# Kernel tuning notes

Hardware: AMD Instinct MI355X
Metric: run time of the kernel (lower is better)

## Reference

```python
import jax, jax.numpy as jnp
import numpy as np
from jax import lax
from jax.scipy.special import erf

EPS = 1e-5
B = 256

def _conv(x, w, stride):
    return lax.conv_general_dilated(x, w, (stride, stride), ((1, 1), (1, 1)),
                                    dimension_numbers=('NCHW', 'OIHW', 'NCHW'))

def lr_conv(x, alpha, betta, bias, stride):
    # Ternary weight distribution (LR-nets): p0 = P(w=0), p1 = P(w=1)
    p0 = jax.nn.sigmoid(alpha)
    p1 = (1.0 - p0) * jax.nn.sigmoid(betta)
    w_mean = 2.0 * p1 + p0 - 1.0          # E[w] = p1 - p_{-1}
    w_var = (1.0 - p0) - w_mean * w_mean  # Var[w] = E[w^2] - E[w]^2
    m = _conv(x, w_mean, stride) + bias[None, :, None, None]
    v = _conv(x * x, w_var, stride)
    return m, v

def sign_prob(m, v):
    # expected sign under CLT Gaussian: 2*Phi(m/sqrt(v)) - 1 = erf(m / sqrt(2 v))
    return erf(m / jnp.sqrt(2.0 * (v + EPS)))

def setup_inputs() -> dict:
    key = jax.random.key(0)
    ks = jax.random.split(key, 32)
    def n(k, shape, s=1.0):
        return jax.random.normal(k, shape, dtype=jnp.float32) * s
    inp = {}
    inp['x'] = n(ks[0], (B, 3, 32, 32))
    shapes = [(128, 3), (128, 128), (256, 128), (256, 256), (512, 256), (512, 512)]
    i = 1
    for li, (co, ci) in enumerate(shapes, start=1):
        inp['a%d' % li] = n(ks[i], (co, ci, 3, 3)); i += 1
        inp['b%d' % li] = n(ks[i], (co, ci, 3, 3)); i += 1
        inp['c%d' % li] = jnp.zeros((co,), jnp.float32)
    inp['bn_gamma'] = jnp.ones((512,), jnp.float32)
    inp['bn_beta'] = jnp.zeros((512,), jnp.float32)
    inp['fc1_w'] = n(ks[20], (1024, 8192), 0.01)
    inp['fc1_b'] = jnp.zeros((1024,), jnp.float32)
    inp['fc2_w'] = n(ks[21], (10, 1024), 0.03)
    inp['fc2_b'] = jnp.zeros((10,), jnp.float32)
    inp['noise6'] = n(ks[22], (B, 512, 4, 4))
    return inp

def reference(x, a1, b1, c1, a2, b2, c2, a3, b3, c3, a4, b4, c4, a5, b5, c5,
              a6, b6, c6, bn_gamma, bn_beta, fc1_w, fc1_b, fc2_w, fc2_b, noise6):
    h = x
    for (a, bt, c, s) in [(a1, b1, c1, 1), (a2, b2, c2, 2), (a3, b3, c3, 1),
                          (a4, b4, c4, 2), (a5, b5, c5, 1)]:
        m, v = lr_conv(h, a, bt, c, s)
        h = sign_prob(m, v)
    m, v = lr_conv(h, a6, b6, c6, 2)          # output_sample=True layer
    z = m + jnp.sqrt(v + EPS) * noise6        # reparameterized Gaussian sample
    mu = jnp.mean(z, axis=(0, 2, 3), keepdims=True)
    var = jnp.var(z, axis=(0, 2, 3), keepdims=True)
    z = bn_gamma[None, :, None, None] * (z - mu) / jnp.sqrt(var + EPS) + bn_beta[None, :, None, None]
    z = jax.nn.relu(z).reshape(z.shape[0], -1)  # [B, 8192]
    z = jax.nn.relu(z @ fc1_w.T + fc1_b)
    return z @ fc2_w.T + fc2_b
```

## Files before the change

### kernel.cpp

```cpp
#include <hip/hip_runtime.h>
#include <hip/hip_bf16.h>
#include <math.h>

#define EPS 1e-5f

typedef __hip_bfloat16 bf16;
typedef short s16x8 __attribute__((ext_vector_type(8)));
typedef float f32x4 __attribute__((ext_vector_type(4)));

constexpr int ilog2c(int v) { return v <= 1 ? 0 : 1 + ilog2c(v >> 1); }

__device__ __forceinline__ float ldin(const void* p, size_t i, int isbf) {
    return isbf ? __bfloat162float(((const bf16*)p)[i]) : ((const float*)p)[i];
}
__device__ __forceinline__ float b2f_bits(short s) {
    unsigned u = ((unsigned)(unsigned short)s) << 16;
    return __builtin_bit_cast(float, u);
}
__device__ __forceinline__ uint4 sqpk4(uint4 u) {
    uint4 r;
    unsigned* up = (unsigned*)&u;
    unsigned* rp = (unsigned*)&r;
#pragma unroll
    for (int k = 0; k < 4; k++) {
        unsigned w = up[k];
        float lo = __builtin_bit_cast(float, w << 16);
        float hi = __builtin_bit_cast(float, w & 0xffff0000u);
        lo *= lo; hi *= hi;
        unsigned ul = __builtin_bit_cast(unsigned, lo) + 0x8000u;
        unsigned uh = __builtin_bit_cast(unsigned, hi) + 0x8000u;
        rp[k] = (ul >> 16) | (uh & 0xffff0000u);
    }
    return r;
}

__device__ __forceinline__ void dma16(const void* g, void* l) {
    __builtin_amdgcn_global_load_lds(
        (const __attribute__((address_space(1))) void*)g,
        (__attribute__((address_space(3))) void*)l, 16, 0, 0);
}

__global__ __launch_bounds__(64) void detect_kernel(const void* __restrict__ x,
                                                    int* __restrict__ flags,
                                                    char* __restrict__ gA,
                                                    char* __restrict__ gB) {
    const unsigned* w = (const unsigned*)x;
    unsigned word = w[threadIdx.x];
    int e = (word >> 23) & 0xFF;
    bool ok = (word == 0u) || (e >= 0x70 && e <= 0x8E);
    unsigned long long m = __ballot(ok);
    if (threadIdx.x == 0) flags[0] = (__popcll(m) >= 32) ? 0 : 1;
    if (threadIdx.x < 16) ((uint4*)gA)[threadIdx.x] = (uint4){0, 0, 0, 0};
    else if (threadIdx.x < 32) ((uint4*)gB)[threadIdx.x - 16] = (uint4){0, 0, 0, 0};
}

__global__ __launch_bounds__(256) void prep_w_l1(
    const void* __restrict__ alpha, const void* __restrict__ betta,
    const int* __restrict__ flags, float* __restrict__ wmv, int n)
{
    int i = blockIdx.x * 256 + threadIdx.x;
    if (i >= n) return;
    int fl = flags[0];
    float a = ldin(alpha, i, fl), b = ldin(betta, i, fl);
    float p0 = 1.f / (1.f + expf(-a));
    float p1 = (1.f - p0) / (1.f + expf(-b));
    float m = 2.f * p1 + p0 - 1.f;
    wmv[i] = m;
    wmv[n + i] = (1.f - p0) - m * m;
}

__global__ __launch_bounds__(256) void prep_w_r(
    const void* __restrict__ alpha, const void* __restrict__ betta,
    const int* __restrict__ flags, bf16* __restrict__ wmr, bf16* __restrict__ wvr,
    int lc, int n)
{
    int o = blockIdx.x * 256 + threadIdx.x;
    if (o >= n) return;
    int fl = flags[0];
    int cotap = o >> lc;
    int ci = o & ((1 << lc) - 1);
    int co = cotap / 9;
    int tap = cotap - co * 9;
    int i = (((co << lc) + ci) * 9) + tap;
    float a = ldin(alpha, i, fl), b = ldin(betta, i, fl);
    float p0 = 1.f / (1.f + expf(-a));
    float p1 = (1.f - p0) / (1.f + expf(-b));
    float m = 2.f * p1 + p0 - 1.f;
    float v = (1.f - p0) - m * m;
    wmr[o] = __float2bfloat16(m);
    wvr[o] = __float2bfloat16(v);
}

__global__ __launch_bounds__(256) void permute_fc1(
    const void* __restrict__ w, const int* __restrict__ flags, bf16* __restrict__ wp)
{
    __shared__ float L[8192];
    const int fl = flags[0];
    int tid = threadIdx.x;
    int o = blockIdx.x;
    size_t srow = (size_t)o * 8192;
    for (int c = tid; c < 512; c += 256) {
        float v[16];
        if (fl) {
            const uint4* s = (const uint4*)((const bf16*)w + srow + c * 16);
            uint4 u0 = s[0], u1 = s[1];
            const unsigned short* h0 = (const unsigned short*)&u0;
            const unsigned short* h1 = (const unsigned short*)&u1;
#pragma unroll
            for (int j = 0; j < 8; j++) { v[j] = b2f_bits((short)h0[j]); v[8 + j] = b2f_bits((short)h1[j]); }
        } else {
            const float4* s = (const float4*)((const float*)w + srow + c * 16);
#pragma unroll
            for (int j = 0; j < 4; j++) {
                float4 t4 = s[j];
                v[j * 4 + 0] = t4.x; v[j * 4 + 1] = t4.y; v[j * 4 + 2] = t4.z; v[j * 4 + 3] = t4.w;
            }
        }
#pragma unroll
        for (int hw = 0; hw < 16; hw++) L[hw * 512 + c] = v[hw];
    }
    __syncthreads();
    for (int j = 0; j < 32; j++) {
        int idx = j * 256 + tid;
        wp[srow + idx] = __float2bfloat16(L[idx]);
    }
}

__global__ __launch_bounds__(256) void l1_conv(
    const void* __restrict__ x, const float* __restrict__ wmv,
    const void* __restrict__ bias, const int* __restrict__ flags,
    bf16* __restrict__ out)
{
    __shared__ float Xs[64][28];
    const int fl = flags[0];
    int tid = threadIdx.x;
    int pos0 = blockIdx.x * 64;
    int b = pos0 >> 10;
    for (int u = tid; u < 576; u += 256) {
        int p = u / 9, r = u - p * 9;
        int ci = r / 3, kh = r - ci * 3;
        int pos = pos0 + p;
        int oh = (pos >> 5) & 31, ow = pos & 31;
        int ih = oh - 1 + kh;
        bool okh = (unsigned)ih < 32u;
        size_t base = ((size_t)(b * 3 + ci) * 32 + ih) * 32;
#pragma unroll
        for (int kw = 0; kw < 3; kw++) {
            int iw = ow - 1 + kw;
            float v = (okh && (unsigned)iw < 32u) ? ldin(x, base + iw, fl) : 0.f;
            Xs[p][ci * 9 + kh * 3 + kw] = v;
        }
    }
    int c = tid & 127, pg = tid >> 7;
    float wm[27], wv[27];
#pragma unroll
    for (int k = 0; k < 27; k++) {
        wm[k] = wmv[c * 27 + k];
        wv[k] = wmv[3456 + c * 27 + k];
    }
    float bs = ldin(bias, c, fl);
    __syncthreads();
    for (int it = 0; it < 32; it++) {
        int p = it * 2 + pg;
        float aM = 0.f, aV = 0.f;
#pragma unroll
        for (int k = 0; k < 27; k++) {
            float xv = Xs[p][k];
            aM = fmaf(xv, wm[k], aM);
            aV = fmaf(xv * xv, wv[k], aV);
        }
        out[(size_t)(pos0 + p) * 128 + c] =
            __float2bfloat16(erff((aM + bs) * rsqrtf(2.f * (aV + EPS))));
    }
}

template<int CI, int CO, int H, int W, int S, int OH, int OW, int ACT, int SQX, int COT>
__global__ __launch_bounds__(256, 2) void conv_gemm(
    const char* __restrict__ xreg,
    int sqoff, int zpoff,
    const bf16* __restrict__ wmr,
    const bf16* __restrict__ wvr,
    const void* __restrict__ bias, const void* __restrict__ noise,
    const int* __restrict__ flags,
    void* __restrict__ outp, bf16* __restrict__ outsq)
{
    constexpr int OHW = OH * OW;
    constexpr int KC = CI / 64;
    constexpr int NC = 9 * KC;
    constexpr int WJ = COT / 32;
    constexpr int NIW = COT / 8;
    constexpr int LOHW = ilog2c(OHW), LOW = ilog2c(OW);
    constexpr int LH = ilog2c(H), LW = ilog2c(W);
    static_assert(COT == 128 || COT == 64, "");

    __shared__ bf16 Xs[128 * 64];
    __shared__ bf16 Xq[128 * 64];
    __shared__ bf16 Wms[COT * 64];
    __shared__ bf16 Wvs[COT * 64];

    const int tid = threadIdx.x;
    const int lane = tid & 63, wv_ = tid >> 6;
    const int q = lane >> 4, l15 = lane & 15;
    const int pw = (wv_ >> 1) * 64, cw = (wv_ & 1) * (16 * WJ);
    const int c0 = blockIdx.y * COT;
    const int bx128 = blockIdx.x * 128;

    const int lrow = lane >> 3;
    const int u16 = (((lane & 7) ^ lrow) << 4);

    const int wlb = ((c0 + lrow) * 9 * CI + (((lane & 7) ^ lrow) << 3)) * 2;

    const bf16* wsrc = (wv_ == 3) ? wvr : wmr;
    bf16* wdst = (wv_ == 3) ? Wvs : Wms;
    bf16* xdst = (wv_ == 1) ? Xq : Xs;
    const int xadd = (wv_ == 1) ? sqoff : 0;

    f32x4 accM[4][WJ], accV[4][WJ];
#pragma unroll
    for (int i = 0; i < 4; i++)
#pragma unroll
        for (int j = 0; j < WJ; j++) {
            accM[i][j] = (f32x4){0.f, 0.f, 0.f, 0.f};
            accV[i][j] = (f32x4){0.f, 0.f, 0.f, 0.f};
        }

    for (int t = 0; t < NC; t++) {
        const int tap = t / KC, ci0 = (t % KC) * 64;
        const int kh = tap / 3, kw = tap - 3 * kh;
        const int sci = ci0 * 2;

        __syncthreads();
        if (wv_ >= 2) {
            const int base = wlb + t * 128;
#pragma unroll
            for (int k = 0; k < NIW; k++)
                dma16((const char*)wsrc + base + k * (8 * 9 * CI * 2),
                      (char*)wdst + k * 1024);
        } else {
            if constexpr (!SQX) {
#pragma unroll
                for (int k = 0; k < 16; k++) {
                    int P = bx128 + 8 * k + lrow;
                    int bi = P >> LOHW;
                    int oh = (P >> LOW) & (OH - 1);
                    int ow = P & (OW - 1);
                    int ih = oh * S - 1 + kh;
                    int iw = ow * S - 1 + kw;
                    bool ok = ((unsigned)ih < (unsigned)H) && ((unsigned)iw < (unsigned)W);
                    int off = ((((bi << LH) + ih) << LW) + iw) * (CI * 2) + u16 + sci + xadd;
                    off = ok ? off : zpoff;
                    dma16(xreg + off, (char*)xdst + k * 1024);
                }
            } else {
#pragma unroll
                for (int ts = 0; ts < 8; ts++) {
                    int k = 2 * ts + wv_;
                    int P = bx128 + 8 * k + lrow;
                    int bi = P >> LOHW;
                    int oh = (P >> LOW) & (OH - 1);
                    int ow = P & (OW - 1);
                    int ih = oh * S - 1 + kh;
                    int iw = ow * S - 1 + kw;
                    bool ok = ((unsigned)ih < (unsigned)H) && ((unsigned)iw < (unsigned)W);
                    int off = ((((bi << LH) + ih) << LW) + iw) * (CI * 2) + u16 + sci;
                    uint4 g = (uint4){0, 0, 0, 0};
                    if (ok) g = *(const uint4*)(xreg + off);
                    *(uint4*)((char*)Xs + k * 1024 + lane * 16) = g;
                    *(uint4*)((char*)Xq + k * 1024 + lane * 16) = sqpk4(g);
                }
            }
        }
        __syncthreads();

#pragma unroll
        for (int ks = 0; ks < 2; ks++) {
            const int pu = (((ks * 4 + q) ^ (l15 & 7)) << 3);
            s16x8 a[4], aq[4];
#pragma unroll
            for (int i = 0; i < 4; i++) {
                const int ra = pw + i * 16 + l15;
                a[i]  = *(const s16x8*)(Xs + ra * 64 + pu);
                aq[i] = *(const s16x8*)(Xq + ra * 64 + pu);
            }
#pragma unroll
            for (int j = 0; j < WJ; j++) {
                const int rb = cw + j * 16 + l15;
                s16x8 bm = *(const s16x8*)(Wms + rb * 64 + pu);
                s16x8 bv = *(const s16x8*)(Wvs + rb * 64 + pu);
#pragma unroll
                for (int i = 0; i < 4; i++) {
                    accM[i][j] = __builtin_amdgcn_mfma_f32_16x16x32_bf16(a[i],  bm, accM[i][j], 0, 0, 0);
                    accV[i][j] = __builtin_amdgcn_mfma_f32_16x16x32_bf16(aq[i], bv, accV[i][j], 0, 0, 0);
                }
            }
        }
    }

    const int fl = flags[0];
#pragma unroll
    for (int j = 0; j < WJ; j++) {
        int co = c0 + cw + j * 16 + l15;
        float bs = ldin(bias, co, fl);
#pragma unroll
        for (int i = 0; i < 4; i++) {
            f32x4 m4 = accM[i][j], v4 = accV[i][j];
#pragma unroll
            for (int r = 0; r < 4; r++) {
                int PP = bx128 + pw + i * 16 + q * 4 + r;
                float mm = m4[r] + bs, vv = v4[r];
                if (ACT == 0) {
                    float y = erff(mm * rsqrtf(2.f * (vv + EPS)));
                    bf16 yb = __float2bfloat16(y);
                    ((bf16*)outp)[(size_t)PP * CO + co] = yb;
                    float yf = __bfloat162float(yb);
                    outsq[(size_t)PP * CO + co] = __float2bfloat16(yf * yf);
                } else {
                    int bb = PP / OHW, hw = PP % OHW;
                    float nz = ldin(noise, ((size_t)bb * CO + co) * OHW + hw, fl);
                    ((float*)outp)[(size_t)PP * CO + co] = mm + sqrtf(vv + EPS) * nz;
                }
            }
        }
    }
}

__global__ __launch_bounds__(256) void fc1_gemm_sk(
    const bf16* __restrict__ A, const bf16* __restrict__ Wp,
    float* __restrict__ part)
{
    __shared__ bf16 Xs[128 * 40];
    __shared__ bf16 Ws[128 * 40];
    int tid = threadIdx.x;
    int lane = tid & 63, wv_ = tid >> 6;
    int q = lane >> 4, l15 = lane & 15;
    const int pw = (wv_ >> 1) * 64, cw = (wv_ & 1) * 64;
    const int p0 = blockIdx.x * 128, c0 = blockIdx.y * 128;
    const int kb = blockIdx.z * 1024;
    const int row_i = tid >> 1, half = tid & 1;

    f32x4 acc[4][4];
#pragma unroll
    for (int i = 0; i < 4; i++)
#pragma unroll
        for (int j = 0; j < 4; j++) acc[i][j] = (f32x4){0.f, 0.f, 0.f, 0.f};

    for (int k0 = kb; k0 < kb + 1024; k0 += 32) {
        __syncthreads();
        {
            const uint4* s = (const uint4*)(A + (size_t)(p0 + row_i) * 8192 + k0 + half * 16);
            uint4* d = (uint4*)(Xs + row_i * 40 + half * 16);
            d[0] = s[0]; d[1] = s[1];
        }
        {
            const uint4* s = (const uint4*)(Wp + (size_t)(c0 + row_i) * 8192 + k0 + half * 16);
            uint4* d = (uint4*)(Ws + row_i * 40 + half * 16);
            d[0] = s[0]; d[1] = s[1];
        }
        __syncthreads();
        s16x8 a[4], bb[4];
#pragma unroll
        for (int i = 0; i < 4; i++) {
            a[i]  = *(const s16x8*)(Xs + (pw + i * 16 + l15) * 40 + q * 8);
            bb[i] = *(const s16x8*)(Ws + (cw + i * 16 + l15) * 40 + q * 8);
        }
#pragma unroll
        for (int i = 0; i < 4; i++)
#pragma unroll
            for (int j = 0; j < 4; j++)
                acc[i][j] = __builtin_amdgcn_mfma_f32_16x16x32_bf16(a[i], bb[j], acc[i][j], 0, 0, 0);
    }

    float* pbase = part + (size_t)blockIdx.z * 256 * 1024;
#pragma unroll
    for (int j = 0; j < 4; j++) {
        int co = c0 + cw + j * 16 + l15;
#pragma unroll
        for (int i = 0; i < 4; i++) {
            f32x4 m4 = acc[i][j];
#pragma unroll
            for (int r = 0; r < 4; r++) {
                int P = p0 + pw + i * 16 + q * 4 + r;
                pbase[(size_t)P * 1024 + co] = m4[r];
            }
        }
    }
}

__global__ __launch_bounds__(256) void fc1_reduce(
    const float* __restrict__ part, const void* __restrict__ bias,
    const int* __restrict__ flags, float* __restrict__ out)
{
    int i = blockIdx.x * 256 + threadIdx.x;
    float s = 0.f;
#pragma unroll
    for (int k = 0; k < 8; k++) s += part[(size_t)k * 262144 + i];
    out[i] = fmaxf(s + ldin(bias, i & 1023, flags[0]), 0.f);
}

__global__ __launch_bounds__(256) void bn_part(const float* __restrict__ z,
                                               float4* __restrict__ partial)
{
    int blk = blockIdx.x;
    int t = threadIdx.x;
    float s0 = 0, ss0 = 0, s1 = 0, ss1 = 0;
    for (int p = 0; p < 32; p++) {
        float2 v = ((const float2*)z)[((size_t)(blk * 32 + p)) * 256 + t];
        s0 += v.x; ss0 += v.x * v.x;
        s1 += v.y; ss1 += v.y * v.y;
    }
    partial[blk * 256 + t] = make_float4(s0, ss0, s1, ss1);
}

__global__ __launch_bounds__(512) void bn_fin(
    const float4* __restrict__ partial, const void* __restrict__ gamma,
    const void* __restrict__ beta, const int* __restrict__ flags,
    float* __restrict__ sc, float* __restrict__ sh)
{
    int c = threadIdx.x;
    float s = 0, ss = 0;
    for (int j = 0; j < 128; j++) {
        float4 pv = partial[j * 256 + (c >> 1)];
        s += (c & 1) ? pv.z : pv.x;
        ss += (c & 1) ? pv.w : pv.y;
    }
    float mean = s * (1.f / 4096.f);
    float var = ss * (1.f / 4096.f) - mean * mean;
    int fl = flags[0];
    float scale = ldin(gamma, c, fl) * rsqrtf(var + EPS);
    sc[c] = scale;
    sh[c] = ldin(beta, c, fl) - mean * scale;
}

__global__ __launch_bounds__(256) void bn_apply(
    const float* __restrict__ z, const float* __restrict__ sc,
    const float* __restrict__ sh, bf16* __restrict__ zr)
{
    int i = blockIdx.x * 256 + threadIdx.x;
    int c = i & 511;
    float v = z[i] * sc[c] + sh[c];
    zr[i] = __float2bfloat16(fmaxf(v, 0.f));
}

__global__ __launch_bounds__(640) void fc2_kernel(
    const float* __restrict__ A, const void* __restrict__ W,
    const void* __restrict__ bias, const int* __restrict__ flags,
    void* __restrict__ out)
{
    const int fl = flags[0];
    int n = blockIdx.x;
    int o = threadIdx.x >> 6;
    int lane = threadIdx.x & 63;
    const float* a = A + (size_t)n * 1024;
    size_t wbase = (size_t)o * 1024;
    float s = 0.f;
    for (int i = lane; i < 1024; i += 64) s = fmaf(a[i], ldin(W, wbase + i, fl), s);
#pragma unroll
    for (int off = 32; off > 0; off >>= 1) s += __shfl_down(s, off);
    if (lane == 0) {
        float v = s + ldin(bias, o, fl);
        if (fl) ((bf16*)out)[n * 10 + o] = __float2bfloat16(v);
        else    ((float*)out)[n * 10 + o] = v;
    }
}

extern "C" void kernel_launch(void* const* d_in, const int* in_sizes, int n_in,
                              void* d_out, int out_size, void* d_ws, size_t ws_size,
                              hipStream_t stream)
{
    const void* x = d_in[0];
    const void *al[6], *be[6], *bi[6];
    for (int l = 0; l < 6; l++) {
        al[l] = d_in[1 + 3 * l];
        be[l] = d_in[2 + 3 * l];
        bi[l] = d_in[3 + 3 * l];
    }
    const void* bn_gamma = d_in[19];
    const void* bn_beta  = d_in[20];
    const void* fc1_w = d_in[21];
    const void* fc1_b = d_in[22];
    const void* fc2_w = d_in[23];
    const void* fc2_b = d_in[24];
    const void* noise = d_in[25];

    char* base = (char*)d_ws;
    size_t off = 0;
    auto alloc = [&](size_t bytes) { void* p = base + off; off += (bytes + 255) & ~(size_t)255; return p; };
    int* flags = (int*)alloc(256);
    float* w1 = (float*)alloc(2 * 3456 * sizeof(float));
    const int SwLC[5] = {7, 7, 8, 8, 9};
    const size_t Sw[5] = {147456, 294912, 589824, 1179648, 2359296};
    bf16 *wmr[5], *wvr[5];
    for (int l = 0; l < 5; l++) {
        wmr[l] = (bf16*)alloc(Sw[l] * sizeof(bf16));
        wvr[l] = (bf16*)alloc(Sw[l] * sizeof(bf16));
    }
    bf16* Wp   = (bf16*)alloc((size_t)1024 * 8192 * sizeof(bf16));
    float4* part = (float4*)alloc((size_t)128 * 256 * sizeof(float4));
    float* bnsc = (float*)alloc(512 * sizeof(float));
    float* bnsh = (float*)alloc(512 * sizeof(float));
    float* fc1o = (float*)alloc((size_t)256 * 1024 * sizeof(float));
    bf16* zr   = (bf16*)alloc((size_t)256 * 8192 * sizeof(bf16));

    const int ZPA = 67108864;
    const int ZPB = 33554432;
    char* RA = (char*)alloc((size_t)ZPA + 256);
    char* RB = (char*)alloc((size_t)ZPB + 256);
    float* z = (float*)RB;
    float* fc1part = (float*)(RB + 8388608);

    detect_kernel<<<1, 64, 0, stream>>>(x, flags, RA + ZPA, RB + ZPB);

    prep_w_l1<<<14, 256, 0, stream>>>(al[0], be[0], flags, w1, 3456);
    for (int l = 0; l < 5; l++) {
        int n = (int)Sw[l];
        prep_w_r<<<(n + 255) / 256, 256, 0, stream>>>(
            al[l + 1], be[l + 1], flags, wmr[l], wvr[l], SwLC[l], n);
    }
    permute_fc1<<<1024, 256, 0, stream>>>(fc1_w, flags, Wp);

    l1_conv<<<4096, 256, 0, stream>>>(x, w1, bi[0], flags, (bf16*)RA);

    conv_gemm<128, 128, 32, 32, 2, 16, 16, 0, 1, 128><<<dim3(512, 1), 256, 0, stream>>>(
        RA, 0, ZPA, wmr[0], wvr[0], bi[1], nullptr, flags,
        RB, (bf16*)(RB + 16777216));
    conv_gemm<128, 256, 16, 16, 1, 16, 16, 0, 0, 128><<<dim3(512, 2), 256, 0, stream>>>(
        RB, 16777216, ZPB, wmr[1], wvr[1], bi[2], nullptr, flags,
        RA, (bf16*)(RA + 33554432));
    conv_gemm<256, 256, 16, 16, 2, 8, 8, 0, 0, 128><<<dim3(128, 2), 256, 0, stream>>>(
        RA, 33554432, ZPA, wmr[2], wvr[2], bi[3], nullptr, flags,
        RB, (bf16*)(RB + 8388608));
    conv_gemm<256, 512, 8, 8, 1, 8, 8, 0, 0, 128><<<dim3(128, 4), 256, 0, stream>>>(
        RB, 8388608, ZPB, wmr[3], wvr[3], bi[4], nullptr, flags,
        RA, (bf16*)(RA + 16777216));
    conv_gemm<512, 512, 8, 8, 2, 4, 4, 1, 0, 64><<<dim3(32, 8), 256, 0, stream>>>(
        RA, 16777216, ZPA, wmr[4], wvr[4], bi[5], noise, flags,
        z, nullptr);

    bn_part<<<128, 256, 0, stream>>>(z, part);
    bn_fin<<<1, 512, 0, stream>>>(part, bn_gamma, bn_beta, flags, bnsc, bnsh);
    bn_apply<<<8192, 256, 0, stream>>>(z, bnsc, bnsh, zr);

    fc1_gemm_sk<<<dim3(2, 8, 8), 256, 0, stream>>>(zr, Wp, fc1part);
    fc1_reduce<<<1024, 256, 0, stream>>>(fc1part, fc1_b, flags, fc1o);
    fc2_kernel<<<256, 640, 0, stream>>>(fc1o, fc2_w, fc2_b, flags, d_out);
}
```

Before: 781.1 us.

## Double-buffer conv GEMM K-chunks and stage activation epilogue through LDS

Makes the conv GEMM K loop use 32-channel chunks with double-buffered LDS, so the next tile's global/DMA loads are issued before computing the current one and one barrier per iteration is removed. Per-row position offsets are precomputed once instead of every chunk. For the erf activation path, outputs are first written to LDS and then stored as coalesced 16-byte rows instead of scattered 2-byte stores. The costs are twice as many loop iterations with half-K MFMA work per barrier, more registers held for prefetch, and the same LDS footprint, which may affect occupancy at two blocks per CU.

```diff
diff --git a/kernel.cpp b/kernel.cpp
--- a/kernel.cpp
+++ b/kernel.cpp
@@ -185,18 +185,22 @@
     void* __restrict__ outp, bf16* __restrict__ outsq)
 {
     constexpr int OHW = OH * OW;
-    constexpr int KC = CI / 64;
+    constexpr int KC = CI / 32;
     constexpr int NC = 9 * KC;
     constexpr int WJ = COT / 32;
-    constexpr int NIW = COT / 8;
+    constexpr int NW = COT / 16;
+    constexpr int XB = 128 * 64;
+    constexpr int WB = COT * 64;
     constexpr int LOHW = ilog2c(OHW), LOW = ilog2c(OW);
     constexpr int LH = ilog2c(H), LW = ilog2c(W);
-    static_assert(COT == 128 || COT == 64, "");
-
-    __shared__ bf16 Xs[128 * 64];
-    __shared__ bf16 Xq[128 * 64];
-    __shared__ bf16 Wms[COT * 64];
-    __shared__ bf16 Wvs[COT * 64];
+    constexpr int SMEM = 4 * XB + 4 * WB;
+    static_assert(ACT == 1 || COT == 128, "LDS epilogue assumes 256B rows");
+
+    __shared__ __align__(16) char smem[SMEM];
+    char* const Xs0 = smem;
+    char* const Xq0 = smem + 2 * XB;
+    char* const Wm0 = smem + 4 * XB;
+    char* const Wv0 = smem + 4 * XB + 2 * WB;
 
     const int tid = threadIdx.x;
     const int lane = tid & 63, wv_ = tid >> 6;
@@ -205,15 +209,19 @@
     const int c0 = blockIdx.y * COT;
     const int bx128 = blockIdx.x * 128;
 
-    const int lrow = lane >> 3;
-    const int u16 = (((lane & 7) ^ lrow) << 4);
-
-    const int wlb = ((c0 + lrow) * 9 * CI + (((lane & 7) ^ lrow) << 3)) * 2;
-
-    const bf16* wsrc = (wv_ == 3) ? wvr : wmr;
-    bf16* wdst = (wv_ == 3) ? Wvs : Wms;
-    bf16* xdst = (wv_ == 1) ? Xq : Xs;
-    const int xadd = (wv_ == 1) ? sqoff : 0;
+    const int lrow = lane >> 2;
+    const int u16 = (((lane & 3) ^ (lrow & 3)) << 4);
+
+    int xb[8], ohS[8], owS[8];
+#pragma unroll
+    for (int k = 0; k < 8; k++) {
+        int P = bx128 + 16 * k + lrow;
+        int bi = P >> LOHW;
+        ohS[k] = ((P >> LOW) & (OH - 1)) * S - 1;
+        owS[k] = (P & (OW - 1)) * S - 1;
+        xb[k] = bi * (H * W * CI * 2);
+    }
+    const int wlb = ((c0 + lrow) * 9 * CI) * 2 + u16;
 
     f32x4 accM[4][WJ], accV[4][WJ];
 #pragma unroll
@@ -224,97 +232,145 @@
             accV[i][j] = (f32x4){0.f, 0.f, 0.f, 0.f};
         }
 
+    uint4 g[4];
+
+    auto stageW = [&](int t, int nb) {
+        const int tap = t / KC, ci = (t - tap * KC) * 32;
+        const char* src = (const char*)((wv_ == 3) ? wvr : wmr) + wlb + (tap * CI + ci) * 2;
+        char* dst = ((wv_ == 3) ? Wv0 : Wm0) + nb * WB;
+#pragma unroll
+        for (int k = 0; k < NW; k++)
+            dma16(src + k * (16 * 9 * CI * 2), dst + k * 1024);
+    };
+
+    auto stageX = [&](int t, int nb) {
+        const int tap = t / KC, ci = (t - tap * KC) * 32;
+        const int kh = tap / 3, kw = tap - 3 * kh;
+        char* dst = ((wv_ == 1) ? Xq0 : Xs0) + nb * XB;
+        const int xadd = (wv_ == 1) ? sqoff : 0;
+#pragma unroll
+        for (int k = 0; k < 8; k++) {
+            int ih = ohS[k] + kh, iw = owS[k] + kw;
+            bool ok = ((unsigned)ih < (unsigned)H) && ((unsigned)iw < (unsigned)W);
+            int off = xb[k] + (ih * W + iw) * (CI * 2) + u16 + ci * 2 + xadd;
+            off = ok ? off : zpoff;
+            dma16(xreg + off, dst + k * 1024);
+        }
+    };
+
+    auto loadX = [&](int t) {
+        const int tap = t / KC, ci = (t - tap * KC) * 32;
+        const int kh = tap / 3, kw = tap - 3 * kh;
+#pragma unroll
+        for (int ts = 0; ts < 4; ts++) {
+            const int k = 2 * ts + wv_;
+            int ih = ohS[k] + kh, iw = owS[k] + kw;
+            bool ok = ((unsigned)ih < (unsigned)H) && ((unsigned)iw < (unsigned)W);
+            int off = xb[k] + (ih * W + iw) * (CI * 2) + u16 + ci * 2;
+            g[ts] = (uint4){0, 0, 0, 0};
+            if (ok) g[ts] = *(const uint4*)(xreg + off);
+        }
+    };
+    auto writeX = [&](int nb) {
+#pragma unroll
+        for (int ts = 0; ts < 4; ts++) {
+            const int k = 2 * ts + wv_;
+            *(uint4*)(Xs0 + nb * XB + k * 1024 + lane * 16) = g[ts];
+            *(uint4*)(Xq0 + nb * XB + k * 1024 + lane * 16) = sqpk4(g[ts]);
+        }
+    };
+
+    auto compute = [&](int nb) {
+        const bf16* Xs = (const bf16*)(Xs0 + nb * XB);
+        const bf16* Xq = (const bf16*)(Xq0 + nb * XB);
+        const bf16* Wm = (const bf16*)(Wm0 + nb * WB);
+        const bf16* Wv = (const bf16*)(Wv0 + nb * WB);
+        const int pu = (q ^ (l15 & 3)) << 3;
+        s16x8 a[4], aq[4];
+#pragma unroll
+        for (int i = 0; i < 4; i++) {
+            const int ra = pw + i * 16 + l15;
+            a[i]  = *(const s16x8*)(Xs + ra * 32 + pu);
+            aq[i] = *(const s16x8*)(Xq + ra * 32 + pu);
+        }
+#pragma unroll
+        for (int j = 0; j < WJ; j++) {
+            const int rb = cw + j * 16 + l15;
+            s16x8 bm = *(const s16x8*)(Wm + rb * 32 + pu);
+            s16x8 bv = *(const s16x8*)(Wv + rb * 32 + pu);
+#pragma unroll
+            for (int i = 0; i < 4; i++) {
+                accM[i][j] = __builtin_amdgcn_mfma_f32_16x16x32_bf16(a[i],  bm, accM[i][j], 0, 0, 0);
+                accV[i][j] = __builtin_amdgcn_mfma_f32_16x16x32_bf16(aq[i], bv, accV[i][j], 0, 0, 0);
+            }
+        }
+    };
+
+    if (wv_ >= 2) stageW(0, 0);
+    else if constexpr (!SQX) stageX(0, 0);
+    else { loadX(0); writeX(0); }
+    __syncthreads();
+
+#pragma unroll 2
     for (int t = 0; t < NC; t++) {
-        const int tap = t / KC, ci0 = (t % KC) * 64;
-        const int kh = tap / 3, kw = tap - 3 * kh;
-        const int sci = ci0 * 2;
-
+        const int cur = t & 1;
+        const bool more = (t + 1 < NC);
+        if (more) {
+            if (wv_ >= 2) stageW(t + 1, cur ^ 1);
+            else if constexpr (!SQX) stageX(t + 1, cur ^ 1);
+            else loadX(t + 1);
+        }
+        compute(cur);
+        if constexpr (SQX) { if (wv_ < 2 && more) writeX(cur ^ 1); }
         __syncthreads();
-        if (wv_ >= 2) {
-            const int base = wlb + t * 128;
-#pragma unroll
-            for (int k = 0; k < NIW; k++)
-                dma16((const char*)wsrc + base + k * (8 * 9 * CI * 2),
-                      (char*)wdst + k * 1024);
-        } else {
-            if constexpr (!SQX) {
-#pragma unroll
-                for (int k = 0; k < 16; k++) {
-                    int P = bx128 + 8 * k + lrow;
-                    int bi = P >> LOHW;
-                    int oh = (P >> LOW) & (OH - 1);
-                    int ow = P & (OW - 1);
-                    int ih = oh * S - 1 + kh;
-                    int iw = ow * S - 1 + kw;
-                    bool ok = ((unsigned)ih < (unsigned)H) && ((unsigned)iw < (unsigned)W);
-                    int off = ((((bi << LH) + ih) << LW) + iw) * (CI * 2) + u16 + sci + xadd;
-                    off = ok ? off : zpoff;
-                    dma16(xreg + off, (char*)xdst + k * 1024);
-                }
-            } else {
-#pragma unroll
-                for (int ts = 0; ts < 8; ts++) {
-                    int k = 2 * ts + wv_;
-                    int P = bx128 + 8 * k + lrow;
-                    int bi = P >> LOHW;
-                    int oh = (P >> LOW) & (OH - 1);
-                    int ow = P & (OW - 1);
-                    int ih = oh * S - 1 + kh;
-                    int iw = ow * S - 1 + kw;
-                    bool ok = ((unsigned)ih < (unsigned)H) && ((unsigned)iw < (unsigned)W);
-                    int off = ((((bi << LH) + ih) << LW) + iw) * (CI * 2) + u16 + sci;
-                    uint4 g = (uint4){0, 0, 0, 0};
-                    if (ok) g = *(const uint4*)(xreg + off);
-                    *(uint4*)((char*)Xs + k * 1024 + lane * 16) = g;
-                    *(uint4*)((char*)Xq + k * 1024 + lane * 16) = sqpk4(g);
+    }
+
+    const int fl = flags[0];
+    if constexpr (ACT == 0) {
+        bf16* Lact = (bf16*)smem;
+        bf16* Lsq  = (bf16*)(smem + 128 * COT * 2);
+#pragma unroll
+        for (int j = 0; j < WJ; j++) {
+            int co = c0 + cw + j * 16 + l15;
+            float bs = ldin(bias, co, fl);
+#pragma unroll
+            for (int i = 0; i < 4; i++) {
+#pragma unroll
+                for (int r = 0; r < 4; r++) {
+                    int PPl = pw + i * 16 + q * 4 + r;
+                    float mm = accM[i][j][r] + bs, vv = accV[i][j][r];
+                    float y = erff(mm * rsqrtf(2.f * (vv + EPS)));
+                    bf16 yb = __float2bfloat16(y);
+                    float yf = __bfloat162float(yb);
+                    int lc = cw + j * 16 + l15;
+                    Lact[PPl * COT + lc] = yb;
+                    Lsq [PPl * COT + lc] = __float2bfloat16(yf * yf);
                 }
             }
         }
         __syncthreads();
-
-#pragma unroll
-        for (int ks = 0; ks < 2; ks++) {
-            const int pu = (((ks * 4 + q) ^ (l15 & 7)) << 3);
-            s16x8 a[4], aq[4];
+#pragma unroll
+        for (int k = 0; k < 8; k++) {
+            int f = k * 4096 + tid * 16;
+            int rowl = f >> 8;
+            int colb = f & 255;
+            uint4 va = *(const uint4*)((char*)Lact + f);
+            uint4 vs = *(const uint4*)((char*)Lsq + f);
+            size_t gb = ((size_t)(bx128 + rowl) * CO + c0) * 2 + colb;
+            *(uint4*)((char*)outp + gb) = va;
+            *(uint4*)((char*)outsq + gb) = vs;
+        }
+    } else {
+#pragma unroll
+        for (int j = 0; j < WJ; j++) {
+            int co = c0 + cw + j * 16 + l15;
+            float bs = ldin(bias, co, fl);
 #pragma unroll
             for (int i = 0; i < 4; i++) {
-                const int ra = pw + i * 16 + l15;
-                a[i]  = *(const s16x8*)(Xs + ra * 64 + pu);
-                aq[i] = *(const s16x8*)(Xq + ra * 64 + pu);
-            }
-#pragma unroll
-            for (int j = 0; j < WJ; j++) {
-                const int rb = cw + j * 16 + l15;
-                s16x8 bm = *(const s16x8*)(Wms + rb * 64 + pu);
-                s16x8 bv = *(const s16x8*)(Wvs + rb * 64 + pu);
-#pragma unroll
-                for (int i = 0; i < 4; i++) {
-                    accM[i][j] = __builtin_amdgcn_mfma_f32_16x16x32_bf16(a[i],  bm, accM[i][j], 0, 0, 0);
-                    accV[i][j] = __builtin_amdgcn_mfma_f32_16x16x32_bf16(aq[i], bv, accV[i][j], 0, 0, 0);
-                }
-            }
-        }
-    }
-
-    const int fl = flags[0];
-#pragma unroll
-    for (int j = 0; j < WJ; j++) {
-        int co = c0 + cw + j * 16 + l15;
-        float bs = ldin(bias, co, fl);
-#pragma unroll
-        for (int i = 0; i < 4; i++) {
-            f32x4 m4 = accM[i][j], v4 = accV[i][j];
-#pragma unroll
-            for (int r = 0; r < 4; r++) {
-                int PP = bx128 + pw + i * 16 + q * 4 + r;
-                float mm = m4[r] + bs, vv = v4[r];
-                if (ACT == 0) {
-                    float y = erff(mm * rsqrtf(2.f * (vv + EPS)));
-                    bf16 yb = __float2bfloat16(y);
-                    ((bf16*)outp)[(size_t)PP * CO + co] = yb;
-                    float yf = __bfloat162float(yb);
-                    outsq[(size_t)PP * CO + co] = __float2bfloat16(yf * yf);
-                } else {
+#pragma unroll
+                for (int r = 0; r < 4; r++) {
+                    int PP = bx128 + pw + i * 16 + q * 4 + r;
+                    float mm = accM[i][j][r] + bs, vv = accV[i][j][r];
                     int bb = PP / OHW, hw = PP % OHW;
                     float nz = ldin(noise, ((size_t)bb * CO + co) * OHW + hw, fl);
                     ((float*)outp)[(size_t)PP * CO + co] = mm + sqrtf(vv + EPS) * nz;
```

After: 755.4 us. 1.03x faster.

## Triple-buffer conv GEMM loads and compute squared activations in registers

Applied to the files above, without the earlier changes.

The conv GEMM now walks the K dimension in 32-channel chunks through a three-stage shared-memory ring. Async DMA of chunk t+2 overlaps MFMA on chunk t, with hand-placed waitcnt/barrier. The separate squared-activation tensor is dropped: x² is computed in registers from the loaded A fragments, which removes the extra global writes and reads of outsq. The activation epilogue is staged through LDS for coalesced 16-byte stores, and layer 3 switches to 64-channel tiles. This trades more LDS and hand-tuned wait counts, which could be fragile, for less memory traffic and better latency hiding.

```diff
diff --git a/kernel.cpp b/kernel.cpp
--- a/kernel.cpp
+++ b/kernel.cpp
@@ -174,29 +174,27 @@
     }
 }
 
-template<int CI, int CO, int H, int W, int S, int OH, int OW, int ACT, int SQX, int COT>
+template<int CI, int CO, int H, int W, int S, int OH, int OW, int ACT, int COT>
 __global__ __launch_bounds__(256, 2) void conv_gemm(
     const char* __restrict__ xreg,
-    int sqoff, int zpoff,
+    int zpoff,
     const bf16* __restrict__ wmr,
     const bf16* __restrict__ wvr,
     const void* __restrict__ bias, const void* __restrict__ noise,
-    const int* __restrict__ flags,
-    void* __restrict__ outp, bf16* __restrict__ outsq)
+    const int* __restrict__ flags, void* __restrict__ outp)
 {
     constexpr int OHW = OH * OW;
-    constexpr int KC = CI / 64;
+    constexpr int KC = CI / 32;
     constexpr int NC = 9 * KC;
     constexpr int WJ = COT / 32;
-    constexpr int NIW = COT / 8;
+    constexpr int NW = COT / 16;
+    constexpr int XB = 128 * 64;
+    constexpr int WB = COT * 64;
+    constexpr int BUFB = XB + 2 * WB;
     constexpr int LOHW = ilog2c(OHW), LOW = ilog2c(OW);
-    constexpr int LH = ilog2c(H), LW = ilog2c(W);
-    static_assert(COT == 128 || COT == 64, "");
-
-    __shared__ bf16 Xs[128 * 64];
-    __shared__ bf16 Xq[128 * 64];
-    __shared__ bf16 Wms[COT * 64];
-    __shared__ bf16 Wvs[COT * 64];
+    static_assert(NC % 3 == 0, "");
+
+    __shared__ __align__(16) char smem[3 * BUFB];
 
     const int tid = threadIdx.x;
     const int lane = tid & 63, wv_ = tid >> 6;
@@ -205,15 +203,26 @@
     const int c0 = blockIdx.y * COT;
     const int bx128 = blockIdx.x * 128;
 
-    const int lrow = lane >> 3;
-    const int u16 = (((lane & 7) ^ lrow) << 4);
-
-    const int wlb = ((c0 + lrow) * 9 * CI + (((lane & 7) ^ lrow) << 3)) * 2;
-
-    const bf16* wsrc = (wv_ == 3) ? wvr : wmr;
-    bf16* wdst = (wv_ == 3) ? Wvs : Wms;
-    bf16* xdst = (wv_ == 1) ? Xq : Xs;
-    const int xadd = (wv_ == 1) ? sqoff : 0;
+    const int sl   = (lane & 7) ^ (lane >> 3);
+    const int row2 = 2 * (lane >> 3) + (sl >> 2);
+    const int u16b = (sl & 3) * 16;
+
+    int xb[4], ohS[4], owS[4];
+#pragma unroll
+    for (int kk = 0; kk < 4; kk++) {
+        int P = bx128 + 16 * ((wv_ & 1) * 4 + kk) + row2;
+        int bi = P >> LOHW;
+        ohS[kk] = ((P >> LOW) & (OH - 1)) * S - 1;
+        owS[kk] = (P & (OW - 1)) * S - 1;
+        xb[kk] = bi * (H * W * CI * 2);
+    }
+    const char* wsb = (const char*)((wv_ == 3) ? wvr : wmr)
+                      + (size_t)(c0 + row2) * (9 * CI * 2) + u16b;
+    const int wdoff = XB + ((wv_ == 3) ? WB : 0);
+
+    const int lA = (l15 >> 1) * 128 + (((((l15 & 1) << 2) | q) ^ (l15 >> 1)) << 4);
+    const int abase = pw * 64 + lA;
+    const int bbase = cw * 64 + lA;
 
     f32x4 accM[4][WJ], accV[4][WJ];
 #pragma unroll
@@ -224,97 +233,111 @@
             accV[i][j] = (f32x4){0.f, 0.f, 0.f, 0.f};
         }
 
-    for (int t = 0; t < NC; t++) {
-        const int tap = t / KC, ci0 = (t % KC) * 64;
-        const int kh = tap / 3, kw = tap - 3 * kh;
-        const int sci = ci0 * 2;
-
-        __syncthreads();
-        if (wv_ >= 2) {
-            const int base = wlb + t * 128;
-#pragma unroll
-            for (int k = 0; k < NIW; k++)
-                dma16((const char*)wsrc + base + k * (8 * 9 * CI * 2),
-                      (char*)wdst + k * 1024);
+    auto stage = [&](int t, int nb) {
+        char* buf = smem + nb * BUFB;
+        if (wv_ < 2) {
+            const int tap = t / KC, kci = (t - tap * KC) * 64;
+            const int kh = tap / 3, kw2 = tap - 3 * kh;
+#pragma unroll
+            for (int kk = 0; kk < 4; kk++) {
+                int ih = ohS[kk] + kh, iw = owS[kk] + kw2;
+                bool ok = ((unsigned)ih < (unsigned)H) && ((unsigned)iw < (unsigned)W);
+                int off = xb[kk] + (ih * W + iw) * (CI * 2) + kci + u16b;
+                off = ok ? off : zpoff;
+                dma16(xreg + off, buf + ((wv_ & 1) * 4 + kk) * 1024);
+            }
         } else {
-            if constexpr (!SQX) {
-#pragma unroll
-                for (int k = 0; k < 16; k++) {
-                    int P = bx128 + 8 * k + lrow;
-                    int bi = P >> LOHW;
-                    int oh = (P >> LOW) & (OH - 1);
-                    int ow = P & (OW - 1);
-                    int ih = oh * S - 1 + kh;
-                    int iw = ow * S - 1 + kw;
-                    bool ok = ((unsigned)ih < (unsigned)H) && ((unsigned)iw < (unsigned)W);
-                    int off = ((((bi << LH) + ih) << LW) + iw) * (CI * 2) + u16 + sci + xadd;
-                    off = ok ? off : zpoff;
-                    dma16(xreg + off, (char*)xdst + k * 1024);
-                }
-            } else {
-#pragma unroll
-                for (int ts = 0; ts < 8; ts++) {
-                    int k = 2 * ts + wv_;
-                    int P = bx128 + 8 * k + lrow;
-                    int bi = P >> LOHW;
-                    int oh = (P >> LOW) & (OH - 1);
-                    int ow = P & (OW - 1);
-                    int ih = oh * S - 1 + kh;
-                    int iw = ow * S - 1 + kw;
-                    bool ok = ((unsigned)ih < (unsigned)H) && ((unsigned)iw < (unsigned)W);
-                    int off = ((((bi << LH) + ih) << LW) + iw) * (CI * 2) + u16 + sci;
-                    uint4 g = (uint4){0, 0, 0, 0};
-                    if (ok) g = *(const uint4*)(xreg + off);
-                    *(uint4*)((char*)Xs + k * 1024 + lane * 16) = g;
-                    *(uint4*)((char*)Xq + k * 1024 + lane * 16) = sqpk4(g);
+            const char* s = wsb + t * 64;
+            char* d = buf + wdoff;
+#pragma unroll
+            for (int k = 0; k < NW; k++)
+                dma16(s + (size_t)k * (16 * 9 * CI * 2), d + k * 1024);
+        }
+    };
+
+    auto compute = [&](int nb) {
+        const char* buf = smem + nb * BUFB;
+        s16x8 a[4], aq[4];
+#pragma unroll
+        for (int i = 0; i < 4; i++) {
+            a[i] = *(const s16x8*)(buf + abase + i * 1024);
+            uint4 u = *(const uint4*)&a[i];
+            uint4 uq = sqpk4(u);
+            aq[i] = *(const s16x8*)&uq;
+        }
+#pragma unroll
+        for (int j = 0; j < WJ; j++) {
+            s16x8 bm = *(const s16x8*)(buf + XB + bbase + j * 1024);
+            s16x8 bv = *(const s16x8*)(buf + XB + WB + bbase + j * 1024);
+#pragma unroll
+            for (int i = 0; i < 4; i++) {
+                accM[i][j] = __builtin_amdgcn_mfma_f32_16x16x32_bf16(a[i],  bm, accM[i][j], 0, 0, 0);
+                accV[i][j] = __builtin_amdgcn_mfma_f32_16x16x32_bf16(aq[i], bv, accV[i][j], 0, 0, 0);
+            }
+        }
+    };
+
+    auto step = [&](int t, int nb, int nb2) {
+        if (t == NC - 1)
+            asm volatile("s_waitcnt vmcnt(0) lgkmcnt(0)\n\ts_barrier" ::: "memory");
+        else if (COT == 128 && wv_ >= 2)
+            asm volatile("s_waitcnt vmcnt(8) lgkmcnt(0)\n\ts_barrier" ::: "memory");
+        else
+            asm volatile("s_waitcnt vmcnt(4) lgkmcnt(0)\n\ts_barrier" ::: "memory");
+        if (t + 2 < NC) stage(t + 2, nb2);
+        compute(nb);
+    };
+
+    stage(0, 0);
+    stage(1, 1);
+    for (int tt = 0; tt < NC; tt += 3) {
+        step(tt, 0, 2);
+        step(tt + 1, 1, 0);
+        step(tt + 2, 2, 1);
+    }
+
+    __syncthreads();
+    const int fl = flags[0];
+    if constexpr (ACT == 0) {
+        bf16* Lact = (bf16*)smem;
+        constexpr int LCB = ilog2c(COT * 2);
+#pragma unroll
+        for (int j = 0; j < WJ; j++) {
+            int co = c0 + cw + j * 16 + l15;
+            float bs = ldin(bias, co, fl);
+#pragma unroll
+            for (int i = 0; i < 4; i++) {
+#pragma unroll
+                for (int r = 0; r < 4; r++) {
+                    int PPl = pw + i * 16 + q * 4 + r;
+                    float mm = accM[i][j][r] + bs, vv = accV[i][j][r];
+                    Lact[PPl * COT + cw + j * 16 + l15] =
+                        __float2bfloat16(erff(mm * rsqrtf(2.f * (vv + EPS))));
                 }
             }
         }
         __syncthreads();
-
-#pragma unroll
-        for (int ks = 0; ks < 2; ks++) {
-            const int pu = (((ks * 4 + q) ^ (l15 & 7)) << 3);
-            s16x8 a[4], aq[4];
+        constexpr int NST = (128 * COT * 2) / 4096;
+#pragma unroll
+        for (int k = 0; k < NST; k++) {
+            int f = k * 4096 + tid * 16;
+            int rowl = f >> LCB;
+            int colb = f & ((COT * 2) - 1);
+            uint4 va = *(const uint4*)((char*)smem + f);
+            size_t gb = ((size_t)(bx128 + rowl) * CO + c0) * 2 + colb;
+            *(uint4*)((char*)outp + gb) = va;
+        }
+    } else {
+#pragma unroll
+        for (int j = 0; j < WJ; j++) {
+            int co = c0 + cw + j * 16 + l15;
+            float bs = ldin(bias, co, fl);
 #pragma unroll
             for (int i = 0; i < 4; i++) {
-                const int ra = pw + i * 16 + l15;
-                a[i]  = *(const s16x8*)(Xs + ra * 64 + pu);
-                aq[i] = *(const s16x8*)(Xq + ra * 64 + pu);
-            }
-#pragma unroll
-            for (int j = 0; j < WJ; j++) {
-                const int rb = cw + j * 16 + l15;
-                s16x8 bm = *(const s16x8*)(Wms + rb * 64 + pu);
-                s16x8 bv = *(const s16x8*)(Wvs + rb * 64 + pu);
-#pragma unroll
-                for (int i = 0; i < 4; i++) {
-                    accM[i][j] = __builtin_amdgcn_mfma_f32_16x16x32_bf16(a[i],  bm, accM[i][j], 0, 0, 0);
-                    accV[i][j] = __builtin_amdgcn_mfma_f32_16x16x32_bf16(aq[i], bv, accV[i][j], 0, 0, 0);
-                }
-            }
-        }
-    }
-
-    const int fl = flags[0];
-#pragma unroll
-    for (int j = 0; j < WJ; j++) {
-        int co = c0 + cw + j * 16 + l15;
-        float bs = ldin(bias, co, fl);
-#pragma unroll
-        for (int i = 0; i < 4; i++) {
-            f32x4 m4 = accM[i][j], v4 = accV[i][j];
-#pragma unroll
-            for (int r = 0; r < 4; r++) {
-                int PP = bx128 + pw + i * 16 + q * 4 + r;
-                float mm = m4[r] + bs, vv = v4[r];
-                if (ACT == 0) {
-                    float y = erff(mm * rsqrtf(2.f * (vv + EPS)));
-                    bf16 yb = __float2bfloat16(y);
-                    ((bf16*)outp)[(size_t)PP * CO + co] = yb;
-                    float yf = __bfloat162float(yb);
-                    outsq[(size_t)PP * CO + co] = __float2bfloat16(yf * yf);
-                } else {
+#pragma unroll
+                for (int r = 0; r < 4; r++) {
+                    int PP = bx128 + pw + i * 16 + q * 4 + r;
+                    float mm = accM[i][j][r] + bs, vv = accV[i][j][r];
                     int bb = PP / OHW, hw = PP % OHW;
                     float nz = ldin(noise, ((size_t)bb * CO + co) * OHW + hw, fl);
                     ((float*)outp)[(size_t)PP * CO + co] = mm + sqrtf(vv + EPS) * nz;
@@ -502,7 +525,7 @@
     bf16* zr   = (bf16*)alloc((size_t)256 * 8192 * sizeof(bf16));
 
     const int ZPA = 67108864;
-    const int ZPB = 33554432;
+    const int ZPB = 16777216;
     char* RA = (char*)alloc((size_t)ZPA + 256);
     char* RB = (char*)alloc((size_t)ZPB + 256);
     float* z = (float*)RB;
@@ -520,21 +543,16 @@
 
     l1_conv<<<4096, 256, 0, stream>>>(x, w1, bi[0], flags, (bf16*)RA);
 
-    conv_gemm<128, 128, 32, 32, 2, 16, 16, 0, 1, 128><<<dim3(512, 1), 256, 0, stream>>>(
-        RA, 0, ZPA, wmr[0], wvr[0], bi[1], nullptr, flags,
-        RB, (bf16*)(RB + 16777216));
-    conv_gemm<128, 256, 16, 16, 1, 16, 16, 0, 0, 128><<<dim3(512, 2), 256, 0, stream>>>(
-        RB, 16777216, ZPB, wmr[1], wvr[1], bi[2], nullptr, flags,
-        RA, (bf16*)(RA + 33554432));
-    conv_gemm<256, 256, 16, 16, 2, 8, 8, 0, 0, 128><<<dim3(128, 2), 256, 0, stream>>>(
-        RA, 33554432, ZPA, wmr[2], wvr[2], bi[3], nullptr, flags,
-        RB, (bf16*)(RB + 8388608));
-    conv_gemm<256, 512, 8, 8, 1, 8, 8, 0, 0, 128><<<dim3(128, 4), 256, 0, stream>>>(
-        RB, 8388608, ZPB, wmr[3], wvr[3], bi[4], nullptr, flags,
-        RA, (bf16*)(RA + 16777216));
-    conv_gemm<512, 512, 8, 8, 2, 4, 4, 1, 0, 64><<<dim3(32, 8), 256, 0, stream>>>(
-        RA, 16777216, ZPA, wmr[4], wvr[4], bi[5], noise, flags,
-        z, nullptr);
+    conv_gemm<128, 128, 32, 32, 2, 16, 16, 0, 128><<<dim3(512, 1), 256, 0, stream>>>(
+        RA, ZPA, wmr[0], wvr[0], bi[1], nullptr, flags, RB);
+    conv_gemm<128, 256, 16, 16, 1, 16, 16, 0, 128><<<dim3(512, 2), 256, 0, stream>>>(
+        RB, ZPB, wmr[1], wvr[1], bi[2], nullptr, flags, RA);
+    conv_gemm<256, 256, 16, 16, 2, 8, 8, 0, 64><<<dim3(128, 4), 256, 0, stream>>>(
+        RA, ZPA, wmr[2], wvr[2], bi[3], nullptr, flags, RB);
+    conv_gemm<256, 512, 8, 8, 1, 8, 8, 0, 128><<<dim3(128, 4), 256, 0, stream>>>(
+        RB, ZPB, wmr[3], wvr[3], bi[4], nullptr, flags, RA);
+    conv_gemm<512, 512, 8, 8, 2, 4, 4, 1, 64><<<dim3(32, 8), 256, 0, stream>>>(
+        RA, ZPA, wmr[4], wvr[4], bi[5], noise, flags, z);
 
     bn_part<<<128, 256, 0, stream>>>(z, part);
     bn_fin<<<1, 512, 0, stream>>>(part, bn_gamma, bn_beta, flags, bnsc, bnsh);
```

Result: faster. 738.0 us (-5.5%).
